# Optimization experiments

Hardware: AMD Instinct MI355X
Metric: run time of the kernel (lower is better)

The kernel has to match this reference:

```python
import jax, jax.numpy as jnp
import numpy as np

B, I, K, C = 4, 512, 512, 64
EPS_LN = 1e-5


def _ln_last2(x):
    # functional layer_norm over the last TWO dims, no affine params
    mu = x.mean(axis=(-2, -1), keepdims=True)
    var = ((x - mu) ** 2).mean(axis=(-2, -1), keepdims=True)
    return (x - mu) / jnp.sqrt(var + EPS_LN)


def setup_inputs() -> dict:
    key = jax.random.key(0)
    k1, k2, k3, k4, k5, k6, k7, k8 = jax.random.split(key, 8)
    V = jax.random.normal(k1, (B, I, C), dtype=jnp.float32)
    Q = jax.random.normal(k2, (B, K, C), dtype=jnp.float32)
    z = jax.random.normal(k3, (B, I, K, C), dtype=jnp.float32)
    z_mask = (jax.random.uniform(k4, (B, I, K)) > 0.3).astype(jnp.float32)
    s = 1.0 / np.sqrt(C)
    W1 = jax.random.normal(k5, (C, C), dtype=jnp.float32) * s
    b1 = jax.random.normal(k6, (C,), dtype=jnp.float32) * 0.01
    W2 = jax.random.normal(k7, (C, C), dtype=jnp.float32) * s
    b2 = jax.random.normal(k8, (C,), dtype=jnp.float32) * 0.01
    return {"V": V, "Q": Q, "z": z, "z_mask": z_mask,
            "W1": W1, "b1": b1, "W2": W2, "b2": b2, "dim": 1}


def reference(V, Q, z, z_mask, W1, b1, W2, b2, dim):
    normalize = True
    # masked exponential normalization along `dim` (per channel c)
    exp_z = jnp.exp(z) * (z_mask[..., None] + 1e-6)          # [b,i,k,c]
    zn = exp_z / exp_z.sum(axis=dim, keepdims=True)
    zn = z_mask[..., None] * zn
    Qa = Q @ W1.T + b1                                       # linear1
    if dim == 1:
        Va = jnp.einsum('bikc,bkc->bic', zn, Qa)
    else:
        Va = jnp.einsum('bikc,bic->bkc', zn, Qa)
    if normalize:
        Va = _ln_last2(Va)
    Vout = V + (Va @ W2.T + b2)                              # linear2 + residual
    if normalize:
        Vout = _ln_last2(Vout)
    return Vout
```

## Files before the change

kernel.cpp:

```cpp
#include <hip/hip_runtime.h>

constexpr int NB = 4;
constexpr int NI = 512;
constexpr int NK = 512;
constexpr int NC = 64;
constexpr float LN_EPS = 1e-5f;

__global__ __launch_bounds__(256) void k_S(const float* __restrict__ z,
                                           const float* __restrict__ zmask,
                                           float* __restrict__ S) {
    int idx = blockIdx.x;
    int ic = idx & 7;  idx >>= 3;
    int kt = idx & 31; int b = idx >> 5;
    int tid = threadIdx.x;
    int kk = tid >> 4;
    int c4 = tid & 15;
    int k = kt * 16 + kk;

    float4 acc = make_float4(0.f, 0.f, 0.f, 0.f);
    for (int ii = 0; ii < NI / 8; ++ii) {
        int i = ic * (NI / 8) + ii;
        size_t row = ((size_t)(b * NI + i) * NK + k) * NC;
        const float4 zv = *(const float4*)(z + row + c4 * 4);
        float m = zmask[(size_t)(b * NI + i) * NK + k] + 1e-6f;
        acc.x += __expf(zv.x) * m;
        acc.y += __expf(zv.y) * m;
        acc.z += __expf(zv.z) * m;
        acc.w += __expf(zv.w) * m;
    }
    float* sp = S + (size_t)(b * NK + k) * NC + c4 * 4;
    atomicAdd(sp + 0, acc.x);
    atomicAdd(sp + 1, acc.y);
    atomicAdd(sp + 2, acc.z);
    atomicAdd(sp + 3, acc.w);
}

__global__ __launch_bounds__(64) void k_R(const float* __restrict__ Q,
                                          const float* __restrict__ W1,
                                          const float* __restrict__ b1,
                                          const float* __restrict__ S,
                                          float* __restrict__ R) {
    int bk = blockIdx.x;
    int c = threadIdx.x;
    __shared__ float q[NC];
    q[c] = Q[(size_t)bk * NC + c];
    __syncthreads();
    const float* w = W1 + c * NC;
    float acc = b1[c];
#pragma unroll
    for (int j = 0; j < NC; ++j) acc += q[j] * w[j];
    R[(size_t)bk * NC + c] = acc / S[(size_t)bk * NC + c];
}

__global__ __launch_bounds__(256) void k_Va(const float* __restrict__ z,
                                            const float* __restrict__ zmask,
                                            const float* __restrict__ R,
                                            float* __restrict__ Va,
                                            float* __restrict__ part1) {
    int bi = blockIdx.x;
    int b = bi >> 9;
    int tid = threadIdx.x;
    int kk = tid >> 4;
    int c4 = tid & 15;

    const float* zrow = z + (size_t)bi * NK * NC;
    const float* mrow = zmask + (size_t)bi * NK;
    const float* Rb = R + (size_t)b * NK * NC;

    float4 acc = make_float4(0.f, 0.f, 0.f, 0.f);
    for (int kb = 0; kb < NK / 16; ++kb) {
        int k = kb * 16 + kk;
        const float4 zv = *(const float4*)(zrow + (size_t)k * NC + c4 * 4);
        const float4 rv = *(const float4*)(Rb + (size_t)k * NC + c4 * 4);
        float zm = mrow[k];
        float m2 = zm * (zm + 1e-6f);
        acc.x += __expf(zv.x) * m2 * rv.x;
        acc.y += __expf(zv.y) * m2 * rv.y;
        acc.z += __expf(zv.z) * m2 * rv.z;
        acc.w += __expf(zv.w) * m2 * rv.w;
    }

    __shared__ float4 part[256];
    part[tid] = acc;
    __syncthreads();
    for (int s = 128; s >= 16; s >>= 1) {
        if (tid < s) {
            float4 o = part[tid + s];
            float4 m = part[tid];
            m.x += o.x; m.y += o.y; m.z += o.z; m.w += o.w;
            part[tid] = m;
        }
        __syncthreads();
    }
    __shared__ float red[32];
    if (tid < 16) {
        float4 v = part[tid];
        *(float4*)(Va + (size_t)bi * NC + tid * 4) = v;
        red[tid]      = v.x + v.y + v.z + v.w;
        red[16 + tid] = v.x * v.x + v.y * v.y + v.z * v.z + v.w * v.w;
    }
    __syncthreads();
    if (tid == 0) {
        float s0 = 0.f, s1 = 0.f;
        for (int t = 0; t < 16; ++t) { s0 += red[t]; s1 += red[16 + t]; }
        part1[bi * 2]     = s0;
        part1[bi * 2 + 1] = s1;
    }
}

__global__ __launch_bounds__(256) void k_red(const float* __restrict__ part,
                                             float* __restrict__ stats) {
    int b = blockIdx.x;
    int tid = threadIdx.x;
    float s0 = 0.f, s1 = 0.f;
    for (int i = tid; i < NI; i += 256) {
        int bi = b * NI + i;
        s0 += part[bi * 2];
        s1 += part[bi * 2 + 1];
    }
    __shared__ float l0[256], l1[256];
    l0[tid] = s0; l1[tid] = s1;
    __syncthreads();
    for (int s = 128; s; s >>= 1) {
        if (tid < s) { l0[tid] += l0[tid + s]; l1[tid] += l1[tid + s]; }
        __syncthreads();
    }
    if (tid == 0) { stats[b * 2] = l0[0]; stats[b * 2 + 1] = l1[0]; }
}

__global__ __launch_bounds__(64) void k_Y(const float* __restrict__ V,
                                          const float* __restrict__ W2,
                                          const float* __restrict__ b2,
                                          const float* __restrict__ Va,
                                          const float* __restrict__ stats1,
                                          float* __restrict__ Y,
                                          float* __restrict__ part2) {
    int bi = blockIdx.x;
    int b = bi >> 9;
    int c = threadIdx.x;
    const float n = (float)(NI * NC);
    float mu = stats1[b * 2] / n;
    float var = stats1[b * 2 + 1] / n - mu * mu;
    float rstd = rsqrtf(var + LN_EPS);

    __shared__ float xn[NC];
    xn[c] = (Va[(size_t)bi * NC + c] - mu) * rstd;
    __syncthreads();

    const float* w = W2 + c * NC;
    float acc = b2[c];
#pragma unroll
    for (int j = 0; j < NC; ++j) acc += xn[j] * w[j];
    float y = V[(size_t)bi * NC + c] + acc;
    Y[(size_t)bi * NC + c] = y;

    float s0 = y, s1 = y * y;
    for (int off = 32; off; off >>= 1) {
        s0 += __shfl_down(s0, off);
        s1 += __shfl_down(s1, off);
    }
    if (c == 0) { part2[bi * 2] = s0; part2[bi * 2 + 1] = s1; }
}

__global__ __launch_bounds__(256) void k_out(const float* __restrict__ Y,
                                             const float* __restrict__ stats2,
                                             float* __restrict__ out) {
    int idx = blockIdx.x * 256 + threadIdx.x;
    int b = idx >> 15;
    const float n = (float)(NI * NC);
    float mu = stats2[b * 2] / n;
    float var = stats2[b * 2 + 1] / n - mu * mu;
    float rstd = rsqrtf(var + LN_EPS);
    out[idx] = (Y[idx] - mu) * rstd;
}

extern "C" void kernel_launch(void* const* d_in, const int* in_sizes, int n_in,
                              void* d_out, int out_size, void* d_ws, size_t ws_size,
                              hipStream_t stream) {
    const float* V  = (const float*)d_in[0];
    const float* Q  = (const float*)d_in[1];
    const float* z  = (const float*)d_in[2];
    const float* zm = (const float*)d_in[3];
    const float* W1 = (const float*)d_in[4];
    const float* b1 = (const float*)d_in[5];
    const float* W2 = (const float*)d_in[6];
    const float* b2 = (const float*)d_in[7];

    float* ws     = (float*)d_ws;
    float* S      = ws;
    float* R      = ws + 131072;
    float* Va     = ws + 262144;
    float* Y      = ws + 393216;
    float* part1  = ws + 524288;
    float* part2  = ws + 528384;
    float* stats1 = ws + 532480;
    float* stats2 = ws + 532488;

    hipMemsetAsync(S, 0, 131072 * sizeof(float), stream);

    k_S  <<<NB * (NK / 16) * 8, 256, 0, stream>>>(z, zm, S);
    k_R  <<<NB * NK,            64,  0, stream>>>(Q, W1, b1, S, R);
    k_Va <<<NB * NI,            256, 0, stream>>>(z, zm, R, Va, part1);
    k_red<<<NB,                 256, 0, stream>>>(part1, stats1);
    k_Y  <<<NB * NI,            64,  0, stream>>>(V, W2, b2, Va, stats1, Y, part2);
    k_red<<<NB,                 256, 0, stream>>>(part2, stats2);
    k_out<<<(NB * NI * NC) / 256, 256, 0, stream>>>(Y, stats2, (float*)d_out);
}
```

Measured before the change: 434.4 us.

## Split z-sum grid finer, dual-accumulate loops, and fold LN stats into atomics

k_S now launches twice as many blocks, each covering 32 rows of i, and both streaming kernels keep two independent accumulators so more loads are in flight per thread. The per-row LayerNorm partial sums are accumulated with global atomics into zeroed stats buffers, which removes both k_red launches and their extra pass over partial arrays. The block reduction in k_Va becomes a single 16-way loop in shared memory plus shuffles instead of a barrier tree. The cost is more atomic traffic on a few addresses per batch and a summation order that no longer gives reproducible results.

Measured after the change: 510.0 us. 1.17x slower.

```diff
diff --git a/kernel.cpp b/kernel.cpp
--- a/kernel.cpp
+++ b/kernel.cpp
@@ -10,29 +10,39 @@
                                            const float* __restrict__ zmask,
                                            float* __restrict__ S) {
     int idx = blockIdx.x;
-    int ic = idx & 7;  idx >>= 3;
+    int ic = idx & 15; idx >>= 4;
     int kt = idx & 31; int b = idx >> 5;
     int tid = threadIdx.x;
     int kk = tid >> 4;
     int c4 = tid & 15;
     int k = kt * 16 + kk;
 
-    float4 acc = make_float4(0.f, 0.f, 0.f, 0.f);
-    for (int ii = 0; ii < NI / 8; ++ii) {
-        int i = ic * (NI / 8) + ii;
-        size_t row = ((size_t)(b * NI + i) * NK + k) * NC;
-        const float4 zv = *(const float4*)(z + row + c4 * 4);
-        float m = zmask[(size_t)(b * NI + i) * NK + k] + 1e-6f;
-        acc.x += __expf(zv.x) * m;
-        acc.y += __expf(zv.y) * m;
-        acc.z += __expf(zv.z) * m;
-        acc.w += __expf(zv.w) * m;
-    }
+    float4 a0 = make_float4(0.f, 0.f, 0.f, 0.f);
+    float4 a1 = make_float4(0.f, 0.f, 0.f, 0.f);
+    for (int ii = 0; ii < 16; ++ii) {
+        int i0 = ic * 32 + ii;
+        int i1 = i0 + 16;
+        size_t r0 = ((size_t)(b * NI + i0) * NK + k) * NC;
+        size_t r1 = ((size_t)(b * NI + i1) * NK + k) * NC;
+        const float4 z0 = *(const float4*)(z + r0 + c4 * 4);
+        const float4 z1 = *(const float4*)(z + r1 + c4 * 4);
+        float m0 = zmask[(size_t)(b * NI + i0) * NK + k] + 1e-6f;
+        float m1 = zmask[(size_t)(b * NI + i1) * NK + k] + 1e-6f;
+        a0.x += __expf(z0.x) * m0;
+        a0.y += __expf(z0.y) * m0;
+        a0.z += __expf(z0.z) * m0;
+        a0.w += __expf(z0.w) * m0;
+        a1.x += __expf(z1.x) * m1;
+        a1.y += __expf(z1.y) * m1;
+        a1.z += __expf(z1.z) * m1;
+        a1.w += __expf(z1.w) * m1;
+    }
+    a0.x += a1.x; a0.y += a1.y; a0.z += a1.z; a0.w += a1.w;
     float* sp = S + (size_t)(b * NK + k) * NC + c4 * 4;
-    atomicAdd(sp + 0, acc.x);
-    atomicAdd(sp + 1, acc.y);
-    atomicAdd(sp + 2, acc.z);
-    atomicAdd(sp + 3, acc.w);
+    atomicAdd(sp + 0, a0.x);
+    atomicAdd(sp + 1, a0.y);
+    atomicAdd(sp + 2, a0.z);
+    atomicAdd(sp + 3, a0.w);
 }
 
 __global__ __launch_bounds__(64) void k_R(const float* __restrict__ Q,
@@ -56,7 +66,7 @@
                                             const float* __restrict__ zmask,
                                             const float* __restrict__ R,
                                             float* __restrict__ Va,
-                                            float* __restrict__ part1) {
+                                            float* __restrict__ stats1) {
     int bi = blockIdx.x;
     int b = bi >> 9;
     int tid = threadIdx.x;
@@ -67,65 +77,50 @@
     const float* mrow = zmask + (size_t)bi * NK;
     const float* Rb = R + (size_t)b * NK * NC;
 
-    float4 acc = make_float4(0.f, 0.f, 0.f, 0.f);
-    for (int kb = 0; kb < NK / 16; ++kb) {
-        int k = kb * 16 + kk;
-        const float4 zv = *(const float4*)(zrow + (size_t)k * NC + c4 * 4);
-        const float4 rv = *(const float4*)(Rb + (size_t)k * NC + c4 * 4);
-        float zm = mrow[k];
-        float m2 = zm * (zm + 1e-6f);
-        acc.x += __expf(zv.x) * m2 * rv.x;
-        acc.y += __expf(zv.y) * m2 * rv.y;
-        acc.z += __expf(zv.z) * m2 * rv.z;
-        acc.w += __expf(zv.w) * m2 * rv.w;
-    }
+    float4 a0 = make_float4(0.f, 0.f, 0.f, 0.f);
+    float4 a1 = make_float4(0.f, 0.f, 0.f, 0.f);
+    for (int kb = 0; kb < 16; ++kb) {
+        int k0 = kb * 16 + kk;
+        int k1 = k0 + 256;
+        const float4 z0 = *(const float4*)(zrow + (size_t)k0 * NC + c4 * 4);
+        const float4 z1 = *(const float4*)(zrow + (size_t)k1 * NC + c4 * 4);
+        const float4 r0 = *(const float4*)(Rb + (size_t)k0 * NC + c4 * 4);
+        const float4 r1 = *(const float4*)(Rb + (size_t)k1 * NC + c4 * 4);
+        float m0 = mrow[k0], mm0 = m0 * (m0 + 1e-6f);
+        float m1 = mrow[k1], mm1 = m1 * (m1 + 1e-6f);
+        a0.x += __expf(z0.x) * mm0 * r0.x;
+        a0.y += __expf(z0.y) * mm0 * r0.y;
+        a0.z += __expf(z0.z) * mm0 * r0.z;
+        a0.w += __expf(z0.w) * mm0 * r0.w;
+        a1.x += __expf(z1.x) * mm1 * r1.x;
+        a1.y += __expf(z1.y) * mm1 * r1.y;
+        a1.z += __expf(z1.z) * mm1 * r1.z;
+        a1.w += __expf(z1.w) * mm1 * r1.w;
+    }
+    a0.x += a1.x; a0.y += a1.y; a0.z += a1.z; a0.w += a1.w;
 
     __shared__ float4 part[256];
-    part[tid] = acc;
+    part[tid] = a0;
     __syncthreads();
-    for (int s = 128; s >= 16; s >>= 1) {
-        if (tid < s) {
-            float4 o = part[tid + s];
-            float4 m = part[tid];
-            m.x += o.x; m.y += o.y; m.z += o.z; m.w += o.w;
-            part[tid] = m;
-        }
-        __syncthreads();
-    }
-    __shared__ float red[32];
     if (tid < 16) {
         float4 v = part[tid];
+#pragma unroll
+        for (int s = 1; s < 16; ++s) {
+            float4 o = part[s * 16 + tid];
+            v.x += o.x; v.y += o.y; v.z += o.z; v.w += o.w;
+        }
         *(float4*)(Va + (size_t)bi * NC + tid * 4) = v;
-        red[tid]      = v.x + v.y + v.z + v.w;
-        red[16 + tid] = v.x * v.x + v.y * v.y + v.z * v.z + v.w * v.w;
-    }
-    __syncthreads();
-    if (tid == 0) {
-        float s0 = 0.f, s1 = 0.f;
-        for (int t = 0; t < 16; ++t) { s0 += red[t]; s1 += red[16 + t]; }
-        part1[bi * 2]     = s0;
-        part1[bi * 2 + 1] = s1;
-    }
-}
-
-__global__ __launch_bounds__(256) void k_red(const float* __restrict__ part,
-                                             float* __restrict__ stats) {
-    int b = blockIdx.x;
-    int tid = threadIdx.x;
-    float s0 = 0.f, s1 = 0.f;
-    for (int i = tid; i < NI; i += 256) {
-        int bi = b * NI + i;
-        s0 += part[bi * 2];
-        s1 += part[bi * 2 + 1];
-    }
-    __shared__ float l0[256], l1[256];
-    l0[tid] = s0; l1[tid] = s1;
-    __syncthreads();
-    for (int s = 128; s; s >>= 1) {
-        if (tid < s) { l0[tid] += l0[tid + s]; l1[tid] += l1[tid + s]; }
-        __syncthreads();
-    }
-    if (tid == 0) { stats[b * 2] = l0[0]; stats[b * 2 + 1] = l1[0]; }
+        float s0 = v.x + v.y + v.z + v.w;
+        float s1 = v.x * v.x + v.y * v.y + v.z * v.z + v.w * v.w;
+        s0 += __shfl_down(s0, 8); s1 += __shfl_down(s1, 8);
+        s0 += __shfl_down(s0, 4); s1 += __shfl_down(s1, 4);
+        s0 += __shfl_down(s0, 2); s1 += __shfl_down(s1, 2);
+        s0 += __shfl_down(s0, 1); s1 += __shfl_down(s1, 1);
+        if (tid == 0) {
+            atomicAdd(&stats1[b * 2],     s0);
+            atomicAdd(&stats1[b * 2 + 1], s1);
+        }
+    }
 }
 
 __global__ __launch_bounds__(64) void k_Y(const float* __restrict__ V,
@@ -134,7 +129,7 @@
                                           const float* __restrict__ Va,
                                           const float* __restrict__ stats1,
                                           float* __restrict__ Y,
-                                          float* __restrict__ part2) {
+                                          float* __restrict__ stats2) {
     int bi = blockIdx.x;
     int b = bi >> 9;
     int c = threadIdx.x;
@@ -159,7 +154,10 @@
         s0 += __shfl_down(s0, off);
         s1 += __shfl_down(s1, off);
     }
-    if (c == 0) { part2[bi * 2] = s0; part2[bi * 2 + 1] = s1; }
+    if (c == 0) {
+        atomicAdd(&stats2[b * 2],     s0);
+        atomicAdd(&stats2[b * 2 + 1], s1);
+    }
 }
 
 __global__ __launch_bounds__(256) void k_out(const float* __restrict__ Y,
@@ -188,21 +186,17 @@
 
     float* ws     = (float*)d_ws;
     float* S      = ws;
-    float* R      = ws + 131072;
-    float* Va     = ws + 262144;
-    float* Y      = ws + 393216;
-    float* part1  = ws + 524288;
-    float* part2  = ws + 528384;
-    float* stats1 = ws + 532480;
-    float* stats2 = ws + 532488;
-
-    hipMemsetAsync(S, 0, 131072 * sizeof(float), stream);
-
-    k_S  <<<NB * (NK / 16) * 8, 256, 0, stream>>>(z, zm, S);
-    k_R  <<<NB * NK,            64,  0, stream>>>(Q, W1, b1, S, R);
-    k_Va <<<NB * NI,            256, 0, stream>>>(z, zm, R, Va, part1);
-    k_red<<<NB,                 256, 0, stream>>>(part1, stats1);
-    k_Y  <<<NB * NI,            64,  0, stream>>>(V, W2, b2, Va, stats1, Y, part2);
-    k_red<<<NB,                 256, 0, stream>>>(part2, stats2);
+    float* stats1 = ws + 131072;
+    float* stats2 = ws + 131080;
+    float* R      = ws + 131088;
+    float* Va     = ws + 262160;
+    float* Y      = ws + 393232;
+
+    hipMemsetAsync(S, 0, (131072 + 16) * sizeof(float), stream);
+
+    k_S  <<<NB * 32 * 16, 256, 0, stream>>>(z, zm, S);
+    k_R  <<<NB * NK,      64,  0, stream>>>(Q, W1, b1, S, R);
+    k_Va <<<NB * NI,      256, 0, stream>>>(z, zm, R, Va, stats1);
+    k_Y  <<<NB * NI,      64,  0, stream>>>(V, W2, b2, Va, stats1, Y, stats2);
     k_out<<<(NB * NI * NC) / 256, 256, 0, stream>>>(Y, stats2, (float*)d_out);
 }
```
